# Performance work log

Measured on AMD Instinct MI355X. Metric: run time of the kernel, lower is better.

## Reference

```python
import jax, jax.numpy as jnp
from jax import lax
import numpy as np

B, T, IN, H, C, L = 128, 80, 4096, 512, 32000, 10


def setup_inputs() -> dict:
    key = jax.random.key(0)
    ks = jax.random.split(key, 19)
    s = 0.05  # param scale for numerical stability
    f = lambda k, shape: (jax.random.normal(k, shape, jnp.float32) * s)
    return {
        "data": jax.random.normal(ks[0], (B, T, IN), jnp.float32),
        "target": jax.random.randint(ks[1], (B, L), 0, C),
        "enc_lin_w": f(ks[2], (H, IN)),
        "enc_lin_b": f(ks[3], (H,)),
        "enc_wih0": f(ks[4], (2, 3 * H, H)),
        "enc_whh0": f(ks[5], (2, 3 * H, H)),
        "enc_bih0": f(ks[6], (2, 3 * H)),
        "enc_bhh0": f(ks[7], (2, 3 * H)),
        "enc_wih1": f(ks[8], (2, 3 * H, 2 * H)),
        "enc_whh1": f(ks[9], (2, 3 * H, H)),
        "enc_bih1": f(ks[10], (2, 3 * H)),
        "enc_bhh1": f(ks[11], (2, 3 * H)),
        "dec_wih": f(ks[12], (3 * H, H)),
        "dec_whh": f(ks[13], (3 * H, H)),
        "dec_bih": f(ks[14], (3 * H,)),
        "dec_bhh": f(ks[15], (3 * H,)),
        "out_w": f(ks[16], (C, 2 * H)),
        "out_b": f(ks[17], (C,)),
        "embed": f(ks[18], (C, H)),
    }


def _gru_cell(x, h, wih, whh, bih, bhh):
    # PyTorch GRU gate math, gates stacked (r, z, n) along 3H.
    gi = x @ wih.T + bih  # (B, 3H)
    gh = h @ whh.T + bhh
    ir, iz, inn = jnp.split(gi, 3, axis=-1)
    hr, hz, hn = jnp.split(gh, 3, axis=-1)
    r = jax.nn.sigmoid(ir + hr)
    z = jax.nn.sigmoid(iz + hz)
    n = jnp.tanh(inn + r * hn)
    return (1.0 - z) * n + z * h


def _gru_layer(x, wih, whh, bih, bhh, reverse):
    # x: (B, T, in) -> outputs (B, T, H), final hidden (B, H)
    h0 = jnp.zeros((x.shape[0], whh.shape[-1]), x.dtype)

    def step(h, xt):
        hn = _gru_cell(xt, h, wih, whh, bih, bhh)
        return hn, hn

    hT, ys = lax.scan(step, h0, jnp.swapaxes(x, 0, 1), reverse=reverse)
    return jnp.swapaxes(ys, 0, 1), hT


def _bidir_layer(x, wih, whh, bih, bhh):
    yf, hf = _gru_layer(x, wih[0], whh[0], bih[0], bhh[0], False)
    yb, hb = _gru_layer(x, wih[1], whh[1], bih[1], bhh[1], True)
    return jnp.concatenate([yf, yb], axis=-1), hf, hb


def reference(data, target, enc_lin_w, enc_lin_b, enc_wih0, enc_whh0, enc_bih0,
              enc_bhh0, enc_wih1, enc_whh1, enc_bih1, enc_bhh1, dec_wih,
              dec_whh, dec_bih, dec_bhh, out_w, out_b, embed):
    # ---- Encoder ----
    x = jax.nn.relu(data @ enc_lin_w.T + enc_lin_b)  # (B, T, H)
    y0, _, _ = _bidir_layer(x, enc_wih0, enc_whh0, enc_bih0, enc_bhh0)
    y1, _, h1b = _bidir_layer(y0, enc_wih1, enc_whh1, enc_bih1, enc_bhh1)
    encode_out = y1[..., :H] + y1[..., H:]  # (B, T, H)
    decode_hid = h1b  # encode_hid[3] = layer-1 backward final hidden (B, H)

    # ---- Decoder loop (teacher forcing; dropout off / eval) ----
    words = target.T  # (L, B)

    def dec_step(h, word):
        emb = embed[word]  # (B, H)
        hn = _gru_cell(emb, h, dec_wih, dec_whh, dec_bih, dec_bhh)
        att = jax.nn.softmax(jnp.einsum('bth,bh->bt', encode_out, hn), axis=1)
        ctx = jnp.einsum('bth,bt->bh', encode_out, att)  # (B, H)
        logits = jnp.concatenate([ctx, hn], axis=-1) @ out_w.T + out_b
        return hn, jax.nn.log_softmax(logits, axis=-1)

    _, logps = lax.scan(dec_step, decode_hid, words)  # (L, B, C)
    pre_prob = jnp.swapaxes(logps, 0, 1)  # (B, L, C)
    pre_sent = jnp.argmax(logps, axis=-1)  # (L, B)
    return pre_prob, pre_sent
```

## Files before the change

### kernel.cpp

```cpp
#include <hip/hip_runtime.h>
#include <cstdint>
#include <cstddef>

#define DEVFN __device__ __forceinline__

DEVFN float sigmf(float x) { return 1.0f / (1.0f + expf(-x)); }

template <int ACT, int RMAP>
__global__ __launch_bounds__(512, 4) void gemm_k(
    const float* __restrict__ A, const float* __restrict__ B,
    const float* __restrict__ bias, float* __restrict__ C, int K, int ldc) {
  constexpr int SST = 132;
  __shared__ float As[2][16 * SST];
  __shared__ float Bs[2][16 * SST];
  const int tid = threadIdx.x;
  const int mA = blockIdx.y * 128;
  const int n0 = blockIdx.x * 128;

  const int sm = tid >> 2;
  const int sq = tid & 3;
  const float* __restrict__ Ap = A + (size_t)(mA + sm) * K + sq * 4;
  const float* __restrict__ Bp = B + (size_t)(n0 + sm) * K + sq * 4;

  const int w = tid >> 6;
  const int lane = tid & 63;
  const int am0 = (w >> 1) * 32 + (lane >> 3) * 4;
  const int bn0 = (w & 1) * 64 + (lane & 7) * 4;

  const float4 fz = {0.f, 0.f, 0.f, 0.f};
  float4 c0a = fz, c0b = fz, c1a = fz, c1b = fz, c2a = fz, c2b = fz,
         c3a = fz, c3b = fz;

#define STAGE_WR(AW, BW, ga, gb)          \
  do {                                    \
    const int kq = sq * 4;                \
    (AW)[(kq + 0) * SST + sm] = (ga).x;   \
    (AW)[(kq + 1) * SST + sm] = (ga).y;   \
    (AW)[(kq + 2) * SST + sm] = (ga).z;   \
    (AW)[(kq + 3) * SST + sm] = (ga).w;   \
    (BW)[(kq + 0) * SST + sm] = (gb).x;   \
    (BW)[(kq + 1) * SST + sm] = (gb).y;   \
    (BW)[(kq + 2) * SST + sm] = (gb).z;   \
    (BW)[(kq + 3) * SST + sm] = (gb).w;   \
  } while (0)

#define FMA8(AV, CA, CB)            \
  CA.x = fmaf(AV, b0.x, CA.x);      \
  CA.y = fmaf(AV, b0.y, CA.y);      \
  CA.z = fmaf(AV, b0.z, CA.z);      \
  CA.w = fmaf(AV, b0.w, CA.w);      \
  CB.x = fmaf(AV, b1.x, CB.x);      \
  CB.y = fmaf(AV, b1.y, CB.y);      \
  CB.z = fmaf(AV, b1.z, CB.z);      \
  CB.w = fmaf(AV, b1.w, CB.w);

#define COMPUTE_TILE(Ab, Bb)                                    \
  _Pragma("unroll") for (int k = 0; k < 16; ++k) {              \
    const float4 av = *(const float4*)&(Ab)[k * SST + am0];     \
    const float4 b0 = *(const float4*)&(Bb)[k * SST + bn0];     \
    const float4 b1 = *(const float4*)&(Bb)[k * SST + bn0 + 32];\
    FMA8(av.x, c0a, c0b)                                        \
    FMA8(av.y, c1a, c1b)                                        \
    FMA8(av.z, c2a, c2b)                                        \
    FMA8(av.w, c3a, c3b)                                        \
  }

  {
    const float4 ga = *(const float4*)Ap;
    const float4 gb = *(const float4*)Bp;
    STAGE_WR(As[0], Bs[0], ga, gb);
  }
  __syncthreads();

  const int nt = K >> 4;
  for (int t = 0; t < nt - 1; ++t) {
    const int kc = (t + 1) << 4;
    const float4 ga = *(const float4*)(Ap + kc);
    const float4 gb = *(const float4*)(Bp + kc);
    const float* __restrict__ Ab = As[t & 1];
    const float* __restrict__ Bb = Bs[t & 1];
    COMPUTE_TILE(Ab, Bb)
    STAGE_WR(As[(t & 1) ^ 1], Bs[(t & 1) ^ 1], ga, gb);
    __syncthreads();
  }
  {
    const float* __restrict__ Ab = As[(nt - 1) & 1];
    const float* __restrict__ Bb = Bs[(nt - 1) & 1];
    COMPUTE_TILE(Ab, Bb)
  }
#undef STAGE_WR
#undef FMA8
#undef COMPUTE_TILE

  const float4 bv0 = *(const float4*)&bias[n0 + bn0];
  const float4 bv1 = *(const float4*)&bias[n0 + bn0 + 32];
#define EPI_ROW(IDX, CA, CB)                                         \
  {                                                                  \
    const int m = mA + am0 + (IDX);                                  \
    int cr;                                                          \
    if (RMAP == 0) cr = m;                                           \
    else if (RMAP == 1) cr = (m % 80) * 128 + m / 80;                \
    else cr = (m & 127) * 10 + (m >> 7);                             \
    float* Cp = C + (size_t)cr * ldc + n0 + bn0;                     \
    float4 o0, o1;                                                   \
    float v;                                                         \
    v = CA.x + bv0.x; o0.x = ACT ? fmaxf(v, 0.f) : v;                \
    v = CA.y + bv0.y; o0.y = ACT ? fmaxf(v, 0.f) : v;                \
    v = CA.z + bv0.z; o0.z = ACT ? fmaxf(v, 0.f) : v;                \
    v = CA.w + bv0.w; o0.w = ACT ? fmaxf(v, 0.f) : v;                \
    v = CB.x + bv1.x; o1.x = ACT ? fmaxf(v, 0.f) : v;                \
    v = CB.y + bv1.y; o1.y = ACT ? fmaxf(v, 0.f) : v;                \
    v = CB.z + bv1.z; o1.z = ACT ? fmaxf(v, 0.f) : v;                \
    v = CB.w + bv1.w; o1.w = ACT ? fmaxf(v, 0.f) : v;                \
    *(float4*)&Cp[0] = o0;                                           \
    *(float4*)&Cp[32] = o1;                                          \
  }
  EPI_ROW(0, c0a, c0b)
  EPI_ROW(1, c1a, c1b)
  EPI_ROW(2, c2a, c2b)
  EPI_ROW(3, c3a, c3b)
#undef EPI_ROW
}

__global__ __launch_bounds__(256, 2) void gru_step_k(
    const float* __restrict__ h_prev, float* __restrict__ h_next,
    const float* __restrict__ gi, int gi_ld, const float* __restrict__ whh,
    const float* __restrict__ bhh, float* __restrict__ y, int y_ld, int i,
    int T) {
  __shared__ float lds_h[32 * 516];
  __shared__ float gh_lds[24 * 33];
  const int tid = threadIdx.x;
  const int jt = blockIdx.x;
  const int bt = blockIdx.y;
  const int d = blockIdx.z;
  const int t_d = (d == 0) ? i : (T - 1 - i);
  const int doff = d * 1536;

  {
    const float* hp = h_prev + ((size_t)(d * 128 + bt * 32)) * 512;
#pragma unroll
    for (int c = 0; c < 16; ++c) {
      const int i4 = c * 256 + tid;
      const int r = i4 >> 7;
      const int k4 = i4 & 127;
      *(float4*)&lds_h[r * 516 + k4 * 4] =
          *(const float4*)&hp[(size_t)r * 512 + k4 * 4];
    }
  }
  __syncthreads();

  const int w = __builtin_amdgcn_readfirstlane(tid >> 6);
  const int lane = tid & 63;
  const int b_loc = lane & 31;
  const int kh = lane >> 5;

  const float* wr[6];
#pragma unroll
  for (int q = 0; q < 6; ++q) {
    const int rl = w * 6 + q;
    const int g = rl >> 3, jh = rl & 7;
    wr[q] = whh + ((size_t)(doff + g * 512 + jt * 8 + jh)) * 512;
  }
  float acc[6] = {0.f, 0.f, 0.f, 0.f, 0.f, 0.f};
  const int kbase = kh * 256;
  for (int k8 = 0; k8 < 256; k8 += 8) {
    const float4 a0 = *(const float4*)&lds_h[b_loc * 516 + kbase + k8];
    const float4 a1 = *(const float4*)&lds_h[b_loc * 516 + kbase + k8 + 4];
#pragma unroll
    for (int q = 0; q < 6; ++q) {
      const float* r_ = wr[q] + kbase + k8;
      acc[q] += r_[0] * a0.x + r_[1] * a0.y + r_[2] * a0.z + r_[3] * a0.w +
                r_[4] * a1.x + r_[5] * a1.y + r_[6] * a1.z + r_[7] * a1.w;
    }
  }
#pragma unroll
  for (int q = 0; q < 6; ++q) acc[q] += __shfl_xor(acc[q], 32);
  if (kh == 0) {
#pragma unroll
    for (int q = 0; q < 6; ++q) gh_lds[(w * 6 + q) * 33 + b_loc] = acc[q];
  }
  __syncthreads();

  const int jh2 = tid & 7;
  const int b2 = tid >> 3;
  const int jg = jt * 8 + jh2;
  const int bg = bt * 32 + b2;
  const float ghr = gh_lds[(jh2) * 33 + b2];
  const float ghz = gh_lds[(8 + jh2) * 33 + b2];
  const float ghn = gh_lds[(16 + jh2) * 33 + b2];
  const float* gir = gi + (size_t)(t_d * 128 + bg) * gi_ld + doff;
  const float g_r = gir[jg];
  const float g_z = gir[512 + jg];
  const float g_n = gir[1024 + jg];
  const float r = sigmf(g_r + ghr + bhh[doff + jg]);
  const float z = sigmf(g_z + ghz + bhh[doff + 512 + jg]);
  const float n = tanhf(g_n + r * (ghn + bhh[doff + 1024 + jg]));
  const float hold = lds_h[b2 * 516 + jg];
  const float hnew = (1.f - z) * n + z * hold;
  h_next[((size_t)(d * 128 + bg)) * 512 + jg] = hnew;
  y[((size_t)(t_d * 128 + bg)) * y_ld + d * 512 + jg] = hnew;
}

__global__ void fold_k(const float* __restrict__ y1, float* __restrict__ eo) {
  const size_t i = (size_t)blockIdx.x * 256 + threadIdx.x;
  const size_t r = i >> 7;
  const int k4 = (int)(i & 127);
  const float* s = y1 + r * 1024 + k4 * 4;
  const float4 a = *(const float4*)s;
  const float4 c = *(const float4*)(s + 512);
  float4 o;
  o.x = a.x + c.x; o.y = a.y + c.y; o.z = a.z + c.z; o.w = a.w + c.w;
  *(float4*)&eo[r * 512 + k4 * 4] = o;
}

__global__ void gather_k(const float* __restrict__ embed,
                         const int* __restrict__ target,
                         float* __restrict__ out) {
  const int rowid = blockIdx.x;
  const int l = rowid >> 7, b = rowid & 127;
  const int wd = target[b * 10 + l];
  const float4* src = (const float4*)(embed + (size_t)wd * 512);
  float4* dst = (float4*)(out + (size_t)rowid * 512);
  dst[threadIdx.x] = src[threadIdx.x];
}

__global__ __launch_bounds__(256) void attn_k(const float* __restrict__ enc,
                                              const float* __restrict__ hn_all,
                                              float* __restrict__ Z) {
  __shared__ float hs[512];
  __shared__ float sc[80];
  __shared__ float att[80];
  const int l = blockIdx.x >> 7;
  const int b = blockIdx.x & 127;
  const int tid = threadIdx.x;
  const size_t hrow = (size_t)(l * 128 + b) * 512;
  if (tid < 128)
    *(float4*)&hs[tid * 4] = *(const float4*)&hn_all[hrow + tid * 4];
  __syncthreads();
  const int w = tid >> 6, lane = tid & 63;
  for (int t = w; t < 80; t += 4) {
    const float* e = enc + ((size_t)(t * 128 + b)) * 512 + lane * 8;
    const float4 e0 = *(const float4*)e;
    const float4 e1 = *(const float4*)(e + 4);
    const float* h8 = &hs[lane * 8];
    float p = e0.x * h8[0] + e0.y * h8[1] + e0.z * h8[2] + e0.w * h8[3] +
              e1.x * h8[4] + e1.y * h8[5] + e1.z * h8[6] + e1.w * h8[7];
#pragma unroll
    for (int off = 1; off < 64; off <<= 1) p += __shfl_xor(p, off);
    if (lane == 0) sc[t] = p;
  }
  __syncthreads();
  if (w == 0) {
    const float v0 = sc[lane];
    const float v1 = (lane < 16) ? sc[64 + lane] : -3.4e38f;
    float m = fmaxf(v0, v1);
#pragma unroll
    for (int off = 1; off < 64; off <<= 1) m = fmaxf(m, __shfl_xor(m, off));
    const float e0 = expf(v0 - m);
    const float e1 = (lane < 16) ? expf(v1 - m) : 0.f;
    float s = e0 + e1;
#pragma unroll
    for (int off = 1; off < 64; off <<= 1) s += __shfl_xor(s, off);
    att[lane] = e0 / s;
    if (lane < 16) att[64 + lane] = e1 / s;
  }
  __syncthreads();
  float c0 = 0.f, c1 = 0.f;
  for (int t = 0; t < 80; ++t) {
    const float* e = enc + ((size_t)(t * 128 + b)) * 512;
    const float a = att[t];
    c0 += a * e[tid];
    c1 += a * e[tid + 256];
  }
  const size_t zr = (size_t)(l * 128 + b) * 1024;
  Z[zr + tid] = c0;
  Z[zr + 256 + tid] = c1;
  Z[zr + 512 + tid] = hs[tid];
  Z[zr + 768 + tid] = hs[256 + tid];
}

__global__ __launch_bounds__(256) void lsm_k(float* __restrict__ out) {
  const int row = blockIdx.x;
  float* p = out + (size_t)row * 32000;
  const int tid = threadIdx.x;
  float bv = -3.4e38f;
  int bi = 0;
  for (int c = 0; c < 125; ++c) {
    const int idx = c * 256 + tid;
    const float v = p[idx];
    if (v > bv || (v == bv && idx < bi)) { bv = v; bi = idx; }
  }
#pragma unroll
  for (int off = 1; off < 64; off <<= 1) {
    const float ov = __shfl_xor(bv, off);
    const int oi = __shfl_xor(bi, off);
    if (ov > bv || (ov == bv && oi < bi)) { bv = ov; bi = oi; }
  }
  __shared__ float wv[4];
  __shared__ int wi[4];
  __shared__ float wsm[4];
  const int w = tid >> 6, lane = tid & 63;
  if (lane == 0) { wv[w] = bv; wi[w] = bi; }
  __syncthreads();
  float m = wv[0];
  int mi = wi[0];
#pragma unroll
  for (int q = 1; q < 4; ++q) {
    if (wv[q] > m || (wv[q] == m && wi[q] < mi)) { m = wv[q]; mi = wi[q]; }
  }
  float s = 0.f;
  for (int c = 0; c < 125; ++c) s += expf(p[c * 256 + tid] - m);
#pragma unroll
  for (int off = 1; off < 64; off <<= 1) s += __shfl_xor(s, off);
  if (lane == 0) wsm[w] = s;
  __syncthreads();
  const float lse = m + logf(wsm[0] + wsm[1] + wsm[2] + wsm[3]);
  for (int c = 0; c < 125; ++c) {
    const int idx = c * 256 + tid;
    p[idx] = p[idx] - lse;
  }
  if (tid == 0) out[40960000 + (row % 10) * 128 + (row / 10)] = (float)mi;
}

extern "C" void kernel_launch(void* const* d_in, const int* in_sizes, int n_in,
                              void* d_out, int out_size, void* d_ws,
                              size_t ws_size, hipStream_t stream) {
  (void)in_sizes; (void)n_in; (void)out_size; (void)ws_size;
  const float* data = (const float*)d_in[0];
  const int* target = (const int*)d_in[1];
  const float* enc_lin_w = (const float*)d_in[2];
  const float* enc_lin_b = (const float*)d_in[3];
  const float* enc_wih0 = (const float*)d_in[4];
  const float* enc_whh0 = (const float*)d_in[5];
  const float* enc_bih0 = (const float*)d_in[6];
  const float* enc_bhh0 = (const float*)d_in[7];
  const float* enc_wih1 = (const float*)d_in[8];
  const float* enc_whh1 = (const float*)d_in[9];
  const float* enc_bih1 = (const float*)d_in[10];
  const float* enc_bhh1 = (const float*)d_in[11];
  const float* dec_wih = (const float*)d_in[12];
  const float* dec_whh = (const float*)d_in[13];
  const float* dec_bih = (const float*)d_in[14];
  const float* dec_bhh = (const float*)d_in[15];
  const float* out_w = (const float*)d_in[16];
  const float* out_b = (const float*)d_in[17];
  const float* embed = (const float*)d_in[18];
  float* outp = (float*)d_out;

  float* ws = (float*)d_ws;
  size_t off = 0;
  float* buf_gi = ws + off;  off += 31457280;
  float* buf_x = ws + off;   off += 5242880;
  float* buf_y0 = ws + off;  off += 10485760;
  float* buf_y1 = ws + off;  off += 10485760;
  float* h_pp0 = ws + off;   off += 131072;
  float* h_pp1 = ws + off;   off += 131072;
  float* dec_pp0 = ws + off; off += 65536;
  float* dec_pp1 = ws + off; off += 65536;
  float* emb_g = ws + off;   off += 655360;
  float* gi_dec = ws + off;  off += 1966080;
  float* hn_all = ws + off;  off += 655360;
  float* Zb = ws + off;      off += 1310720;

  gemm_k<1, 1><<<dim3(4, 80), 512, 0, stream>>>(data, enc_lin_w, enc_lin_b,
                                                buf_x, 4096, 512);
  gemm_k<0, 0><<<dim3(24, 80), 512, 0, stream>>>(buf_x, enc_wih0, enc_bih0,
                                                 buf_gi, 512, 3072);
  hipMemsetAsync(h_pp0, 0, 2 * 128 * 512 * sizeof(float), stream);
  for (int i = 0; i < 80; ++i) {
    float* hin = (i & 1) ? h_pp1 : h_pp0;
    float* hout = (i & 1) ? h_pp0 : h_pp1;
    gru_step_k<<<dim3(64, 4, 2), 256, 0, stream>>>(
        hin, hout, buf_gi, 3072, enc_whh0, enc_bhh0, buf_y0, 1024, i, 80);
  }
  gemm_k<0, 0><<<dim3(24, 80), 512, 0, stream>>>(buf_y0, enc_wih1, enc_bih1,
                                                 buf_gi, 1024, 3072);
  hipMemsetAsync(h_pp0, 0, 2 * 128 * 512 * sizeof(float), stream);
  for (int i = 0; i < 80; ++i) {
    float* hin = (i & 1) ? h_pp1 : h_pp0;
    float* hout = (i & 1) ? h_pp0 : h_pp1;
    gru_step_k<<<dim3(64, 4, 2), 256, 0, stream>>>(
        hin, hout, buf_gi, 3072, enc_whh1, enc_bhh1, buf_y1, 1024, i, 80);
  }
  fold_k<<<5120, 256, 0, stream>>>(buf_y1, buf_x);
  gather_k<<<1280, 128, 0, stream>>>(embed, target, emb_g);
  gemm_k<0, 0><<<dim3(12, 10), 512, 0, stream>>>(emb_g, dec_wih, dec_bih,
                                                 gi_dec, 512, 1536);
  for (int l = 0; l < 10; ++l) {
    float* hin = (l == 0) ? (h_pp0 + 128 * 512) : ((l & 1) ? dec_pp1 : dec_pp0);
    float* hout = (l & 1) ? dec_pp0 : dec_pp1;
    gru_step_k<<<dim3(64, 4, 1), 256, 0, stream>>>(
        hin, hout, gi_dec, 1536, dec_whh, dec_bhh, hn_all, 512, l, 10);
  }
  attn_k<<<1280, 256, 0, stream>>>(buf_x, hn_all, Zb);
  gemm_k<0, 2><<<dim3(250, 10), 512, 0, stream>>>(Zb, out_w, out_b, outp, 1024,
                                                  32000);
  lsm_k<<<1280, 256, 0, stream>>>(outp);
}
```

Baseline: 7.677 ms.

## Run GRU recurrences as persistent cooperative kernels with grid-wide sync

Replaces the 80 per-timestep GRU launches per encoder layer, and the 10 decoder launches, with one cooperative kernel per recurrence. Each kernel loops over timesteps and calls grid.sync between them. The per-block tile changes to 32 hidden units by 16 batch rows with 512 threads, and the zero-initial hidden state is written into LDS instead of being cleared with a memset. This aims to remove the per-step launch overhead. In exchange it needs every block resident at once (256 blocks, one per CU), pays for a grid barrier every step, and falls back to per-step launches if the cooperative launch fails.

```diff
diff --git a/kernel.cpp b/kernel.cpp
--- a/kernel.cpp
+++ b/kernel.cpp
@@ -1,4 +1,5 @@
 #include <hip/hip_runtime.h>
+#include <hip/hip_cooperative_groups.h>
 #include <cstdint>
 #include <cstddef>
 
@@ -122,72 +123,82 @@
 #undef EPI_ROW
 }
 
-__global__ __launch_bounds__(256, 2) void gru_step_k(
-    const float* __restrict__ h_prev, float* __restrict__ h_next,
-    const float* __restrict__ gi, int gi_ld, const float* __restrict__ whh,
-    const float* __restrict__ bhh, float* __restrict__ y, int y_ld, int i,
-    int T) {
-  __shared__ float lds_h[32 * 516];
-  __shared__ float gh_lds[24 * 33];
-  const int tid = threadIdx.x;
-  const int jt = blockIdx.x;
-  const int bt = blockIdx.y;
-  const int d = blockIdx.z;
-  const int t_d = (d == 0) ? i : (T - 1 - i);
+DEVFN void gru_body(float* lds_h, float* gh_lds, int tid, int jt, int bt,
+                    int d, int i, int T, const float* hsrc, float* hdst,
+                    const float* __restrict__ gi, int gi_ld,
+                    const float* __restrict__ whh,
+                    const float* __restrict__ bhh, float* __restrict__ y,
+                    int y_ld) {
   const int doff = d * 1536;
-
-  {
-    const float* hp = h_prev + ((size_t)(d * 128 + bt * 32)) * 512;
-#pragma unroll
-    for (int c = 0; c < 16; ++c) {
-      const int i4 = c * 256 + tid;
-      const int r = i4 >> 7;
-      const int k4 = i4 & 127;
+  const int j0 = jt * 32;
+  const int b0 = bt * 16;
+
+  if (hsrc) {
+    const float* hp = hsrc + ((size_t)(d * 128 + b0)) * 512;
+#pragma unroll
+    for (int c = 0; c < 4; ++c) {
+      const int i4 = c * 512 + tid;
+      const int r = i4 >> 7, k4 = i4 & 127;
       *(float4*)&lds_h[r * 516 + k4 * 4] =
           *(const float4*)&hp[(size_t)r * 512 + k4 * 4];
     }
-  }
-  __syncthreads();
-
-  const int w = __builtin_amdgcn_readfirstlane(tid >> 6);
+  } else {
+    const float4 z4 = {0.f, 0.f, 0.f, 0.f};
+#pragma unroll
+    for (int c = 0; c < 4; ++c) {
+      const int i4 = c * 512 + tid;
+      const int r = i4 >> 7, k4 = i4 & 127;
+      *(float4*)&lds_h[r * 516 + k4 * 4] = z4;
+    }
+  }
+  __syncthreads();
+
+  const int w = tid >> 6;
   const int lane = tid & 63;
-  const int b_loc = lane & 31;
-  const int kh = lane >> 5;
-
-  const float* wr[6];
-#pragma unroll
-  for (int q = 0; q < 6; ++q) {
-    const int rl = w * 6 + q;
-    const int g = rl >> 3, jh = rl & 7;
-    wr[q] = whh + ((size_t)(doff + g * 512 + jt * 8 + jh)) * 512;
-  }
-  float acc[6] = {0.f, 0.f, 0.f, 0.f, 0.f, 0.f};
-  const int kbase = kh * 256;
-  for (int k8 = 0; k8 < 256; k8 += 8) {
-    const float4 a0 = *(const float4*)&lds_h[b_loc * 516 + kbase + k8];
-    const float4 a1 = *(const float4*)&lds_h[b_loc * 516 + kbase + k8 + 4];
-#pragma unroll
-    for (int q = 0; q < 6; ++q) {
-      const float* r_ = wr[q] + kbase + k8;
+  const int b_loc = lane & 15;
+  const int kh = lane >> 4;
+  const int kbase = kh * 128;
+
+  const float* wr[12];
+#pragma unroll
+  for (int q = 0; q < 12; ++q) {
+    const int rl = w * 12 + q;
+    const int g = rl >> 5, jh = rl & 31;
+    wr[q] = whh + ((size_t)(doff + g * 512 + j0 + jh)) * 512 + kbase;
+  }
+  float acc[12];
+#pragma unroll
+  for (int q = 0; q < 12; ++q) acc[q] = 0.f;
+  const float* hrow = &lds_h[b_loc * 516 + kbase];
+  for (int k8 = 0; k8 < 128; k8 += 8) {
+    const float4 a0 = *(const float4*)&hrow[k8];
+    const float4 a1 = *(const float4*)&hrow[k8 + 4];
+#pragma unroll
+    for (int q = 0; q < 12; ++q) {
+      const float* r_ = wr[q] + k8;
       acc[q] += r_[0] * a0.x + r_[1] * a0.y + r_[2] * a0.z + r_[3] * a0.w +
                 r_[4] * a1.x + r_[5] * a1.y + r_[6] * a1.z + r_[7] * a1.w;
     }
   }
 #pragma unroll
-  for (int q = 0; q < 6; ++q) acc[q] += __shfl_xor(acc[q], 32);
+  for (int q = 0; q < 12; ++q) {
+    acc[q] += __shfl_xor(acc[q], 16);
+    acc[q] += __shfl_xor(acc[q], 32);
+  }
   if (kh == 0) {
 #pragma unroll
-    for (int q = 0; q < 6; ++q) gh_lds[(w * 6 + q) * 33 + b_loc] = acc[q];
-  }
-  __syncthreads();
-
-  const int jh2 = tid & 7;
-  const int b2 = tid >> 3;
-  const int jg = jt * 8 + jh2;
-  const int bg = bt * 32 + b2;
-  const float ghr = gh_lds[(jh2) * 33 + b2];
-  const float ghz = gh_lds[(8 + jh2) * 33 + b2];
-  const float ghn = gh_lds[(16 + jh2) * 33 + b2];
+    for (int q = 0; q < 12; ++q) gh_lds[(w * 12 + q) * 17 + b_loc] = acc[q];
+  }
+  __syncthreads();
+
+  const int jh2 = tid & 31;
+  const int b2 = tid >> 5;
+  const int jg = j0 + jh2;
+  const int bg = b0 + b2;
+  const int t_d = (d == 0) ? i : (T - 1 - i);
+  const float ghr = gh_lds[(jh2) * 17 + b2];
+  const float ghz = gh_lds[(32 + jh2) * 17 + b2];
+  const float ghn = gh_lds[(64 + jh2) * 17 + b2];
   const float* gir = gi + (size_t)(t_d * 128 + bg) * gi_ld + doff;
   const float g_r = gir[jg];
   const float g_z = gir[512 + jg];
@@ -197,8 +208,59 @@
   const float n = tanhf(g_n + r * (ghn + bhh[doff + 1024 + jg]));
   const float hold = lds_h[b2 * 516 + jg];
   const float hnew = (1.f - z) * n + z * hold;
-  h_next[((size_t)(d * 128 + bg)) * 512 + jg] = hnew;
+  hdst[((size_t)(d * 128 + bg)) * 512 + jg] = hnew;
   y[((size_t)(t_d * 128 + bg)) * y_ld + d * 512 + jg] = hnew;
+}
+
+__global__ __launch_bounds__(512, 1) void gru_seq_k(
+    const float* h_init, float* hb0, float* hb1, const float* __restrict__ gi,
+    int gi_ld, const float* __restrict__ whh, const float* __restrict__ bhh,
+    float* __restrict__ y, int y_ld, int T) {
+  cooperative_groups::grid_group grid = cooperative_groups::this_grid();
+  __shared__ float lds_h[16 * 516];
+  __shared__ float gh_lds[96 * 17];
+  const int tid = threadIdx.x;
+  const int jt = blockIdx.x, bt = blockIdx.y, d = blockIdx.z;
+  for (int i = 0; i < T; ++i) {
+    const float* hsrc = (i == 0) ? h_init : ((i & 1) ? hb1 : hb0);
+    float* hdst = (i & 1) ? hb0 : hb1;
+    gru_body(lds_h, gh_lds, tid, jt, bt, d, i, T, hsrc, hdst, gi, gi_ld, whh,
+             bhh, y, y_ld);
+    if (i + 1 < T) {
+      __threadfence();
+      grid.sync();
+      __threadfence();
+    }
+  }
+}
+
+__global__ __launch_bounds__(512, 1) void gru_step2_k(
+    const float* h_prev, float* h_next, const float* __restrict__ gi,
+    int gi_ld, const float* __restrict__ whh, const float* __restrict__ bhh,
+    float* __restrict__ y, int y_ld, int i, int T) {
+  __shared__ float lds_h[16 * 516];
+  __shared__ float gh_lds[96 * 17];
+  gru_body(lds_h, gh_lds, threadIdx.x, blockIdx.x, blockIdx.y, blockIdx.z, i,
+           T, h_prev, h_next, gi, gi_ld, whh, bhh, y, y_ld);
+}
+
+static void run_gru(const float* h_init, float* hb0, float* hb1,
+                    const float* gi, int gi_ld, const float* whh,
+                    const float* bhh, float* y, int y_ld, int T, int D,
+                    hipStream_t stream) {
+  void* args[] = {(void*)&h_init, (void*)&hb0, (void*)&hb1, (void*)&gi,
+                  (void*)&gi_ld,  (void*)&whh, (void*)&bhh, (void*)&y,
+                  (void*)&y_ld,   (void*)&T};
+  hipError_t e = hipLaunchCooperativeKernel((void*)gru_seq_k, dim3(16, 8, D),
+                                            dim3(512, 1, 1), args, 0, stream);
+  if (e != hipSuccess) {
+    for (int i = 0; i < T; ++i) {
+      const float* hs = (i == 0) ? h_init : ((i & 1) ? hb1 : hb0);
+      float* hd = (i & 1) ? hb0 : hb1;
+      gru_step2_k<<<dim3(16, 8, D), dim3(512, 1, 1), 0, stream>>>(
+          hs, hd, gi, gi_ld, whh, bhh, y, y_ld, i, T);
+    }
+  }
 }
 
 __global__ void fold_k(const float* __restrict__ y1, float* __restrict__ eo) {
@@ -366,32 +428,19 @@
                                                 buf_x, 4096, 512);
   gemm_k<0, 0><<<dim3(24, 80), 512, 0, stream>>>(buf_x, enc_wih0, enc_bih0,
                                                  buf_gi, 512, 3072);
-  hipMemsetAsync(h_pp0, 0, 2 * 128 * 512 * sizeof(float), stream);
-  for (int i = 0; i < 80; ++i) {
-    float* hin = (i & 1) ? h_pp1 : h_pp0;
-    float* hout = (i & 1) ? h_pp0 : h_pp1;
-    gru_step_k<<<dim3(64, 4, 2), 256, 0, stream>>>(
-        hin, hout, buf_gi, 3072, enc_whh0, enc_bhh0, buf_y0, 1024, i, 80);
-  }
+  run_gru(nullptr, h_pp0, h_pp1, buf_gi, 3072, enc_whh0, enc_bhh0, buf_y0,
+          1024, 80, 2, stream);
   gemm_k<0, 0><<<dim3(24, 80), 512, 0, stream>>>(buf_y0, enc_wih1, enc_bih1,
                                                  buf_gi, 1024, 3072);
-  hipMemsetAsync(h_pp0, 0, 2 * 128 * 512 * sizeof(float), stream);
-  for (int i = 0; i < 80; ++i) {
-    float* hin = (i & 1) ? h_pp1 : h_pp0;
-    float* hout = (i & 1) ? h_pp0 : h_pp1;
-    gru_step_k<<<dim3(64, 4, 2), 256, 0, stream>>>(
-        hin, hout, buf_gi, 3072, enc_whh1, enc_bhh1, buf_y1, 1024, i, 80);
-  }
+  run_gru(nullptr, h_pp0, h_pp1, buf_gi, 3072, enc_whh1, enc_bhh1, buf_y1,
+          1024, 80, 2, stream);
   fold_k<<<5120, 256, 0, stream>>>(buf_y1, buf_x);
   gather_k<<<1280, 128, 0, stream>>>(embed, target, emb_g);
   gemm_k<0, 0><<<dim3(12, 10), 512, 0, stream>>>(emb_g, dec_wih, dec_bih,
                                                  gi_dec, 512, 1536);
-  for (int l = 0; l < 10; ++l) {
-    float* hin = (l == 0) ? (h_pp0 + 128 * 512) : ((l & 1) ? dec_pp1 : dec_pp0);
-    float* hout = (l & 1) ? dec_pp0 : dec_pp1;
-    gru_step_k<<<dim3(64, 4, 1), 256, 0, stream>>>(
-        hin, hout, gi_dec, 1536, dec_whh, dec_bhh, hn_all, 512, l, 10);
-  }
+  const float* dec_h0 = h_pp0 + 128 * 512;
+  run_gru(dec_h0, dec_pp0, dec_pp1, gi_dec, 1536, dec_whh, dec_bhh, hn_all,
+          512, 10, 1, stream);
   attn_k<<<1280, 256, 0, stream>>>(buf_x, hn_all, Zb);
   gemm_k<0, 2><<<dim3(250, 10), 512, 0, stream>>>(Zb, out_w, out_b, outp, 1024,
                                                   32000);
```

Result: slower. 23.89 ms (+211.2%).

## Split GRU step over 16-row batch tiles with 4-way K split

Applied to the files above, without the earlier changes.

The recurrent GRU step kernel now handles 16 batch rows per block instead of 32, doubling the grid to 64x8 blocks. The K reduction is split four ways with two cross-lane shuffles, and launch bounds are raised to allow more resident blocks. The gi and bias loads are hoisted ahead of the h load and barrier so their latency overlaps. The goal is more parallelism and occupancy in the latency-bound per-timestep kernel, at the cost of reading each W_hh slice from more blocks and leaving half the threads idle in the gate epilogue.

```diff
diff --git a/kernel.cpp b/kernel.cpp
--- a/kernel.cpp
+++ b/kernel.cpp
@@ -122,83 +122,98 @@
 #undef EPI_ROW
 }
 
-__global__ __launch_bounds__(256, 2) void gru_step_k(
+__global__ __launch_bounds__(256, 4) void gru_step_k(
     const float* __restrict__ h_prev, float* __restrict__ h_next,
     const float* __restrict__ gi, int gi_ld, const float* __restrict__ whh,
     const float* __restrict__ bhh, float* __restrict__ y, int y_ld, int i,
     int T) {
-  __shared__ float lds_h[32 * 516];
-  __shared__ float gh_lds[24 * 33];
+  __shared__ float lds_h[16 * 516];
+  __shared__ float gh_lds[24 * 17];
   const int tid = threadIdx.x;
   const int jt = blockIdx.x;
   const int bt = blockIdx.y;
   const int d = blockIdx.z;
   const int t_d = (d == 0) ? i : (T - 1 - i);
   const int doff = d * 1536;
+  const int j0 = jt * 8;
+  const int b0 = bt * 16;
+
+  const int jh2 = tid & 7;
+  const int b2g = tid >> 3;
+  float g_r = 0.f, g_z = 0.f, g_n = 0.f, bh_r = 0.f, bh_z = 0.f, bh_n = 0.f;
+  if (b2g < 16) {
+    const float* gir =
+        gi + (size_t)(t_d * 128 + b0 + b2g) * gi_ld + doff + j0 + jh2;
+    g_r = gir[0];
+    g_z = gir[512];
+    g_n = gir[1024];
+    bh_r = bhh[doff + j0 + jh2];
+    bh_z = bhh[doff + 512 + j0 + jh2];
+    bh_n = bhh[doff + 1024 + j0 + jh2];
+  }
 
   {
-    const float* hp = h_prev + ((size_t)(d * 128 + bt * 32)) * 512;
-#pragma unroll
-    for (int c = 0; c < 16; ++c) {
+    const float* hp = h_prev + ((size_t)(d * 128 + b0)) * 512;
+#pragma unroll
+    for (int c = 0; c < 8; ++c) {
       const int i4 = c * 256 + tid;
-      const int r = i4 >> 7;
-      const int k4 = i4 & 127;
+      const int r = i4 >> 7, k4 = i4 & 127;
       *(float4*)&lds_h[r * 516 + k4 * 4] =
           *(const float4*)&hp[(size_t)r * 512 + k4 * 4];
     }
   }
   __syncthreads();
 
-  const int w = __builtin_amdgcn_readfirstlane(tid >> 6);
+  const int w = tid >> 6;
   const int lane = tid & 63;
-  const int b_loc = lane & 31;
-  const int kh = lane >> 5;
+  const int b_loc = lane & 15;
+  const int kh = lane >> 4;
+  const int kbase = kh * 128;
 
   const float* wr[6];
 #pragma unroll
   for (int q = 0; q < 6; ++q) {
     const int rl = w * 6 + q;
     const int g = rl >> 3, jh = rl & 7;
-    wr[q] = whh + ((size_t)(doff + g * 512 + jt * 8 + jh)) * 512;
+    wr[q] = whh + ((size_t)(doff + g * 512 + j0 + jh)) * 512 + kbase;
   }
   float acc[6] = {0.f, 0.f, 0.f, 0.f, 0.f, 0.f};
-  const int kbase = kh * 256;
-  for (int k8 = 0; k8 < 256; k8 += 8) {
-    const float4 a0 = *(const float4*)&lds_h[b_loc * 516 + kbase + k8];
-    const float4 a1 = *(const float4*)&lds_h[b_loc * 516 + kbase + k8 + 4];
+  const float* hrow = &lds_h[b_loc * 516 + kbase];
+  for (int k8 = 0; k8 < 128; k8 += 8) {
+    const float4 a0 = *(const float4*)&hrow[k8];
+    const float4 a1 = *(const float4*)&hrow[k8 + 4];
 #pragma unroll
     for (int q = 0; q < 6; ++q) {
-      const float* r_ = wr[q] + kbase + k8;
+      const float* r_ = wr[q] + k8;
       acc[q] += r_[0] * a0.x + r_[1] * a0.y + r_[2] * a0.z + r_[3] * a0.w +
                 r_[4] * a1.x + r_[5] * a1.y + r_[6] * a1.z + r_[7] * a1.w;
     }
   }
 #pragma unroll
-  for (int q = 0; q < 6; ++q) acc[q] += __shfl_xor(acc[q], 32);
+  for (int q = 0; q < 6; ++q) {
+    acc[q] += __shfl_xor(acc[q], 16);
+    acc[q] += __shfl_xor(acc[q], 32);
+  }
   if (kh == 0) {
 #pragma unroll
-    for (int q = 0; q < 6; ++q) gh_lds[(w * 6 + q) * 33 + b_loc] = acc[q];
-  }
-  __syncthreads();
-
-  const int jh2 = tid & 7;
-  const int b2 = tid >> 3;
-  const int jg = jt * 8 + jh2;
-  const int bg = bt * 32 + b2;
-  const float ghr = gh_lds[(jh2) * 33 + b2];
-  const float ghz = gh_lds[(8 + jh2) * 33 + b2];
-  const float ghn = gh_lds[(16 + jh2) * 33 + b2];
-  const float* gir = gi + (size_t)(t_d * 128 + bg) * gi_ld + doff;
-  const float g_r = gir[jg];
-  const float g_z = gir[512 + jg];
-  const float g_n = gir[1024 + jg];
-  const float r = sigmf(g_r + ghr + bhh[doff + jg]);
-  const float z = sigmf(g_z + ghz + bhh[doff + 512 + jg]);
-  const float n = tanhf(g_n + r * (ghn + bhh[doff + 1024 + jg]));
-  const float hold = lds_h[b2 * 516 + jg];
-  const float hnew = (1.f - z) * n + z * hold;
-  h_next[((size_t)(d * 128 + bg)) * 512 + jg] = hnew;
-  y[((size_t)(t_d * 128 + bg)) * y_ld + d * 512 + jg] = hnew;
+    for (int q = 0; q < 6; ++q) gh_lds[(w * 6 + q) * 17 + b_loc] = acc[q];
+  }
+  __syncthreads();
+
+  if (b2g < 16) {
+    const float ghr = gh_lds[jh2 * 17 + b2g];
+    const float ghz = gh_lds[(8 + jh2) * 17 + b2g];
+    const float ghn = gh_lds[(16 + jh2) * 17 + b2g];
+    const int jg = j0 + jh2;
+    const int bg = b0 + b2g;
+    const float r = sigmf(g_r + ghr + bh_r);
+    const float z = sigmf(g_z + ghz + bh_z);
+    const float n = tanhf(g_n + r * (ghn + bh_n));
+    const float hold = lds_h[b2g * 516 + jg];
+    const float hnew = (1.f - z) * n + z * hold;
+    h_next[((size_t)(d * 128 + bg)) * 512 + jg] = hnew;
+    y[((size_t)(t_d * 128 + bg)) * y_ld + d * 512 + jg] = hnew;
+  }
 }
 
 __global__ void fold_k(const float* __restrict__ y1, float* __restrict__ eo) {
@@ -370,7 +385,7 @@
   for (int i = 0; i < 80; ++i) {
     float* hin = (i & 1) ? h_pp1 : h_pp0;
     float* hout = (i & 1) ? h_pp0 : h_pp1;
-    gru_step_k<<<dim3(64, 4, 2), 256, 0, stream>>>(
+    gru_step_k<<<dim3(64, 8, 2), 256, 0, stream>>>(
         hin, hout, buf_gi, 3072, enc_whh0, enc_bhh0, buf_y0, 1024, i, 80);
   }
   gemm_k<0, 0><<<dim3(24, 80), 512, 0, stream>>>(buf_y0, enc_wih1, enc_bih1,
@@ -379,7 +394,7 @@
   for (int i = 0; i < 80; ++i) {
     float* hin = (i & 1) ? h_pp1 : h_pp0;
     float* hout = (i & 1) ? h_pp0 : h_pp1;
-    gru_step_k<<<dim3(64, 4, 2), 256, 0, stream>>>(
+    gru_step_k<<<dim3(64, 8, 2), 256, 0, stream>>>(
         hin, hout, buf_gi, 3072, enc_whh1, enc_bhh1, buf_y1, 1024, i, 80);
   }
   fold_k<<<5120, 256, 0, stream>>>(buf_y1, buf_x);
@@ -389,7 +404,7 @@
   for (int l = 0; l < 10; ++l) {
     float* hin = (l == 0) ? (h_pp0 + 128 * 512) : ((l & 1) ? dec_pp1 : dec_pp0);
     float* hout = (l & 1) ? dec_pp0 : dec_pp1;
-    gru_step_k<<<dim3(64, 4, 1), 256, 0, stream>>>(
+    gru_step_k<<<dim3(64, 8, 1), 256, 0, stream>>>(
         hin, hout, gi_dec, 1536, dec_whh, dec_bhh, hn_all, 512, l, 10);
   }
   attn_k<<<1280, 256, 0, stream>>>(buf_x, hn_all, Zb);
```

Measured after the change: 7.654 ms. Within noise of the previous version (-0.3%).
